# Performance work log

Measured on AMD Instinct MI355X. Metric: run time of the kernel, lower is better.

The kernel has to match this reference:

```python
import jax, jax.numpy as jnp
import numpy as np


def setup_inputs() -> dict:
    key = jax.random.key(0)
    k1, k2 = jax.random.split(key)
    B, C, H, W = 4, 32, 512, 512
    inp = jax.random.normal(k1, (B, C, H, W), dtype=jnp.float32)
    # flow displacements of a few pixels, realistic for optical-flow warping
    flow = jax.random.normal(k2, (B, 2, H, W), dtype=jnp.float32) * 8.0
    return {"input": inp, "flow": flow}


def reference(input, flow):
    B, C, H, W = input.shape
    dt = input.dtype
    # meshgrid: grid[:,0]=x coords, grid[:,1]=y coords
    gx = jnp.arange(W, dtype=dt)[None, None, :]          # [1,1,W]
    gy = jnp.arange(H, dtype=dt)[None, :, None]          # [1,H,1]
    x = jnp.clip(gx + flow[:, 0], 0.0, W - 1).reshape(-1)  # [B*H*W]
    y = jnp.clip(gy + flow[:, 1], 0.0, H - 1).reshape(-1)

    x0f = jnp.floor(x)
    y0f = jnp.floor(y)
    x1f = x0f + 1.0
    y1f = y0f + 1.0
    x0 = x0f.astype(jnp.int32)
    y0 = y0f.astype(jnp.int32)
    x1 = jnp.clip(x1f, 0.0, W - 1).astype(jnp.int32)
    y1 = jnp.clip(y1f, 0.0, H - 1).astype(jnp.int32)

    base = jnp.repeat(jnp.arange(B, dtype=jnp.int32) * (H * W), H * W)
    base_y0 = base + y0 * W
    base_y1 = base + y1 * W

    img_flat = jnp.transpose(input, (0, 2, 3, 1)).reshape(-1, C)  # [B*H*W, C]
    Ia = img_flat[base_y0 + x0]
    Ib = img_flat[base_y1 + x0]
    Ic = img_flat[base_y0 + x1]
    Id = img_flat[base_y1 + x1]

    # bilinear weights (note: weights use unclamped x1f/y1f, matching original)
    wa = ((x1f - x) * (y1f - y))[:, None]
    wb = ((x1f - x) * (y - y0f))[:, None]
    wc = ((x - x0f) * (y1f - y))[:, None]
    wd = ((x - x0f) * (y - y0f))[:, None]

    out = wa * Ia + wb * Ib + wc * Ic + wd * Id            # [B*H*W, C]
    return jnp.transpose(out.reshape(B, H, W, C), (0, 3, 1, 2))
```

## Files before the change

### kernel.cpp

```cpp
#include <hip/hip_runtime.h>


constexpr int B = 4, C = 32, H = 512, W = 512;
constexpr int HW = H * W;
constexpr int TILE = 64;
constexpr int APRON = 31;
constexpr int RH = 128;
constexpr int RW = 128;
constexpr int BUF = RH * RW;

__global__ __launch_bounds__(1024, 1) void warp_tile_kernel(
    const float* __restrict__ input,
    const float* __restrict__ flow,
    float* __restrict__ out)
{
    __shared__ float s[2 * BUF];

    int bid0 = (int)blockIdx.x;
    int bid = (bid0 & 7) * 32 + (bid0 >> 3);

    int tx = bid & 7;
    int ty = (bid >> 3) & 7;
    int b  = bid >> 6;
    int tx0 = tx * TILE, ty0 = ty * TILE;

    int rx0 = tx0 - 32;
    int ry0 = ty0 - APRON;

    int tid  = (int)threadIdx.x;
    int lane = tid & 63;
    int wv   = tid >> 6;
    int cl   = tid & 63;
    int rl   = tid >> 6;

    int soff0, soff1, soff2, soff3;
    int ldst0, ldst1, ldst2, ldst3;
    {
        int lrow = lane >> 5;
        int lc   = (lane & 31) << 2;
        int gcol = min(max(rx0 + lc, 0), W - 4);
        int r0 = 8 * wv;
        int g0r = min(max(ry0 + r0 + 0 + lrow, 0), H - 1);
        int g1r = min(max(ry0 + r0 + 2 + lrow, 0), H - 1);
        int g2r = min(max(ry0 + r0 + 4 + lrow, 0), H - 1);
        int g3r = min(max(ry0 + r0 + 6 + lrow, 0), H - 1);
        soff0 = g0r * W + gcol;  ldst0 = (r0 + 0) * RW + 4 * lane;
        soff1 = g1r * W + gcol;  ldst1 = (r0 + 2) * RW + 4 * lane;
        soff2 = g2r * W + gcol;  ldst2 = (r0 + 4) * RW + 4 * lane;
        soff3 = g3r * W + gcol;  ldst3 = (r0 + 6) * RW + 4 * lane;
    }

    float wa[4], wb_[4], wc_[4], wd_[4];
    int a0[4], a1[4];
    int opix0 = (ty0 + rl) * W + tx0 + cl;

    #pragma unroll
    for (int p = 0; p < 4; ++p) {
        int h = ty0 + rl + 16 * p;
        int w = tx0 + cl;
        int pix = h * W + w;
        float fx = flow[(b * 2 + 0) * HW + pix];
        float fy = flow[(b * 2 + 1) * HW + pix];
        float x = fminf(fmaxf((float)w + fx, 0.0f), (float)(W - 1));
        float y = fminf(fmaxf((float)h + fy, 0.0f), (float)(H - 1));
        float x0f = floorf(x), y0f = floorf(y);
        int x0 = (int)x0f, y0 = (int)y0f;
        int y1 = min(y0 + 1, H - 1);
        float dx = x - x0f, dy = y - y0f;
        wa[p]  = (1.f - dx) * (1.f - dy);
        wb_[p] = (1.f - dx) * dy;
        wc_[p] = dx * (1.f - dy);
        wd_[p] = dx * dy;
        int ax0 = x0 - rx0, ay0 = y0 - ry0, ay1 = y1 - ry0;
        bool inreg = (ax0 >= 0) && (ax0 <= RW - 2) && (ay0 >= 0) && (ay1 <= RH - 1);
        a0[p] = inreg ? (ay0 * RW + ax0) : -1;
        a1[p] = ay1 * RW + ax0;
    }

    const float* iplane = input + (size_t)b * C * HW;
    float* oplane = out + (size_t)b * C * HW;

    float4 g0, g1, g2, g3;
    {
        const float* gc = iplane;
        g0 = *(const float4*)(gc + soff0);
        g1 = *(const float4*)(gc + soff1);
        g2 = *(const float4*)(gc + soff2);
        g3 = *(const float4*)(gc + soff3);
        *(float4*)(&s[ldst0]) = g0;
        *(float4*)(&s[ldst1]) = g1;
        *(float4*)(&s[ldst2]) = g2;
        *(float4*)(&s[ldst3]) = g3;
    }
    __syncthreads();

    for (int c = 0; c < C; ++c) {
        if (c + 1 < C) {
            const float* gc = iplane + (size_t)(c + 1) * HW;
            g0 = *(const float4*)(gc + soff0);
            g1 = *(const float4*)(gc + soff1);
            g2 = *(const float4*)(gc + soff2);
            g3 = *(const float4*)(gc + soff3);
        }
        __builtin_amdgcn_sched_barrier(0);

        int base = (c & 1) * BUF;
        float v[4];
        #pragma unroll
        for (int p = 0; p < 4; ++p) {
            if (a0[p] >= 0) {
                int i0 = base + a0[p], i1 = base + a1[p];
                float v00 = s[i0], v01 = s[i0 + 1];
                float v10 = s[i1], v11 = s[i1 + 1];
                v[p] = wa[p] * v00 + wc_[p] * v01 + wb_[p] * v10 + wd_[p] * v11;
            } else {
                int h = ty0 + rl + 16 * p;
                int w = tx0 + cl;
                int pix = h * W + w;
                float fx = flow[(b * 2 + 0) * HW + pix];
                float fy = flow[(b * 2 + 1) * HW + pix];
                float x = fminf(fmaxf((float)w + fx, 0.0f), (float)(W - 1));
                float y = fminf(fmaxf((float)h + fy, 0.0f), (float)(H - 1));
                float x0f = floorf(x), y0f = floorf(y);
                int x0 = (int)x0f, y0 = (int)y0f;
                int x1 = min(x0 + 1, W - 1), y1 = min(y0 + 1, H - 1);
                float dx = x - x0f, dy = y - y0f;
                const float* pch = iplane + (size_t)c * HW;
                v[p] = (1.f - dx) * (1.f - dy) * pch[y0 * W + x0]
                     + (1.f - dx) * dy         * pch[y1 * W + x0]
                     + dx * (1.f - dy)         * pch[y0 * W + x1]
                     + dx * dy                 * pch[y1 * W + x1];
            }
        }

        float* oc = oplane + (size_t)c * HW;
        #pragma unroll
        for (int p = 0; p < 4; ++p)
            oc[opix0 + 16 * p * W] = v[p];

        if (c + 1 < C) {
            int wbase = ((c + 1) & 1) * BUF;
            *(float4*)(&s[wbase + ldst0]) = g0;
            *(float4*)(&s[wbase + ldst1]) = g1;
            *(float4*)(&s[wbase + ldst2]) = g2;
            *(float4*)(&s[wbase + ldst3]) = g3;
            asm volatile("s_waitcnt lgkmcnt(0)" ::: "memory");
            __builtin_amdgcn_sched_barrier(0);
            __builtin_amdgcn_s_barrier();
            __builtin_amdgcn_sched_barrier(0);
        }
    }
}

extern "C" void kernel_launch(void* const* d_in, const int* in_sizes, int n_in,
                              void* d_out, int out_size, void* d_ws, size_t ws_size,
                              hipStream_t stream) {
    const float* input = (const float*)d_in[0];
    const float* flow  = (const float*)d_in[1];
    float* out = (float*)d_out;

    int grid = B * (H / TILE) * (W / TILE);
    warp_tile_kernel<<<grid, 1024, 0, stream>>>(input, flow, out);
}
```

Before: 248.4 us.

## Pack channel pairs as fp16 in shared memory, halving barrier count

Stores two channels per 32-bit LDS word as packed half2, so each staged region covers two channels and the loop processes channel pairs, halving the number of block barriers and LDS reads per channel. Global loads for the next pair are issued before compute, giving more loads in flight. Converting input to fp16 reduces precision of the sampled values, which may exceed tolerance, and adds conversion ALU work and register pressure.

```diff
diff --git a/kernel.cpp b/kernel.cpp
--- a/kernel.cpp
+++ b/kernel.cpp
@@ -1,4 +1,5 @@
 #include <hip/hip_runtime.h>
+#include <hip/hip_fp16.h>
 
 
 constexpr int B = 4, C = 32, H = 512, W = 512;
@@ -9,12 +10,22 @@
 constexpr int RW = 128;
 constexpr int BUF = RH * RW;
 
+static __device__ __forceinline__ float2 h2f(unsigned int u) {
+    __half2 h; __builtin_memcpy(&h, &u, 4);
+    return __half22float2(h);
+}
+static __device__ __forceinline__ unsigned int f2h(float a, float b) {
+    __half2 h = __floats2half2_rn(a, b);
+    unsigned int u; __builtin_memcpy(&u, &h, 4);
+    return u;
+}
+
 __global__ __launch_bounds__(1024, 1) void warp_tile_kernel(
     const float* __restrict__ input,
     const float* __restrict__ flow,
     float* __restrict__ out)
 {
-    __shared__ float s[2 * BUF];
+    __shared__ unsigned int s[2 * BUF];
 
     int bid0 = (int)blockIdx.x;
     int bid = (bid0 & 7) * 32 + (bid0 >> 3);
@@ -80,39 +91,50 @@
     const float* iplane = input + (size_t)b * C * HW;
     float* oplane = out + (size_t)b * C * HW;
 
-    float4 g0, g1, g2, g3;
+    float4 ga0, ga1, ga2, ga3, gb0, gb1, gb2, gb3;
     {
-        const float* gc = iplane;
-        g0 = *(const float4*)(gc + soff0);
-        g1 = *(const float4*)(gc + soff1);
-        g2 = *(const float4*)(gc + soff2);
-        g3 = *(const float4*)(gc + soff3);
-        *(float4*)(&s[ldst0]) = g0;
-        *(float4*)(&s[ldst1]) = g1;
-        *(float4*)(&s[ldst2]) = g2;
-        *(float4*)(&s[ldst3]) = g3;
+        const float* gA = iplane;
+        const float* gB = iplane + HW;
+        ga0 = *(const float4*)(gA + soff0);  gb0 = *(const float4*)(gB + soff0);
+        ga1 = *(const float4*)(gA + soff1);  gb1 = *(const float4*)(gB + soff1);
+        ga2 = *(const float4*)(gA + soff2);  gb2 = *(const float4*)(gB + soff2);
+        ga3 = *(const float4*)(gA + soff3);  gb3 = *(const float4*)(gB + soff3);
+        *(uint4*)(&s[ldst0]) = make_uint4(f2h(ga0.x, gb0.x), f2h(ga0.y, gb0.y),
+                                          f2h(ga0.z, gb0.z), f2h(ga0.w, gb0.w));
+        *(uint4*)(&s[ldst1]) = make_uint4(f2h(ga1.x, gb1.x), f2h(ga1.y, gb1.y),
+                                          f2h(ga1.z, gb1.z), f2h(ga1.w, gb1.w));
+        *(uint4*)(&s[ldst2]) = make_uint4(f2h(ga2.x, gb2.x), f2h(ga2.y, gb2.y),
+                                          f2h(ga2.z, gb2.z), f2h(ga2.w, gb2.w));
+        *(uint4*)(&s[ldst3]) = make_uint4(f2h(ga3.x, gb3.x), f2h(ga3.y, gb3.y),
+                                          f2h(ga3.z, gb3.z), f2h(ga3.w, gb3.w));
     }
     __syncthreads();
 
-    for (int c = 0; c < C; ++c) {
-        if (c + 1 < C) {
-            const float* gc = iplane + (size_t)(c + 1) * HW;
-            g0 = *(const float4*)(gc + soff0);
-            g1 = *(const float4*)(gc + soff1);
-            g2 = *(const float4*)(gc + soff2);
-            g3 = *(const float4*)(gc + soff3);
+    for (int r = 0; r < C / 2; ++r) {
+        int c = 2 * r;
+
+        if (r + 1 < C / 2) {
+            const float* gA = iplane + (size_t)(c + 2) * HW;
+            const float* gB = gA + HW;
+            ga0 = *(const float4*)(gA + soff0);  gb0 = *(const float4*)(gB + soff0);
+            ga1 = *(const float4*)(gA + soff1);  gb1 = *(const float4*)(gB + soff1);
+            ga2 = *(const float4*)(gA + soff2);  gb2 = *(const float4*)(gB + soff2);
+            ga3 = *(const float4*)(gA + soff3);  gb3 = *(const float4*)(gB + soff3);
         }
         __builtin_amdgcn_sched_barrier(0);
 
-        int base = (c & 1) * BUF;
-        float v[4];
+        int base = (r & 1) * BUF;
+        float v0[4], v1[4];
         #pragma unroll
         for (int p = 0; p < 4; ++p) {
             if (a0[p] >= 0) {
                 int i0 = base + a0[p], i1 = base + a1[p];
-                float v00 = s[i0], v01 = s[i0 + 1];
-                float v10 = s[i1], v11 = s[i1 + 1];
-                v[p] = wa[p] * v00 + wc_[p] * v01 + wb_[p] * v10 + wd_[p] * v11;
+                unsigned int d00 = s[i0], d01 = s[i0 + 1];
+                unsigned int d10 = s[i1], d11 = s[i1 + 1];
+                float2 t00 = h2f(d00), t01 = h2f(d01);
+                float2 t10 = h2f(d10), t11 = h2f(d11);
+                v0[p] = wa[p]*t00.x + wc_[p]*t01.x + wb_[p]*t10.x + wd_[p]*t11.x;
+                v1[p] = wa[p]*t00.y + wc_[p]*t01.y + wb_[p]*t10.y + wd_[p]*t11.y;
             } else {
                 int h = ty0 + rl + 16 * p;
                 int w = tx0 + cl;
@@ -125,25 +147,36 @@
                 int x0 = (int)x0f, y0 = (int)y0f;
                 int x1 = min(x0 + 1, W - 1), y1 = min(y0 + 1, H - 1);
                 float dx = x - x0f, dy = y - y0f;
-                const float* pch = iplane + (size_t)c * HW;
-                v[p] = (1.f - dx) * (1.f - dy) * pch[y0 * W + x0]
-                     + (1.f - dx) * dy         * pch[y1 * W + x0]
-                     + dx * (1.f - dy)         * pch[y0 * W + x1]
-                     + dx * dy                 * pch[y1 * W + x1];
+                const float* pc0 = iplane + (size_t)c * HW;
+                const float* pc1 = pc0 + HW;
+                float A = (1.f - dx) * (1.f - dy), Bw = (1.f - dx) * dy;
+                float Cw = dx * (1.f - dy),        Dw = dx * dy;
+                v0[p] = A*pc0[y0*W+x0] + Bw*pc0[y1*W+x0]
+                      + Cw*pc0[y0*W+x1] + Dw*pc0[y1*W+x1];
+                v1[p] = A*pc1[y0*W+x0] + Bw*pc1[y1*W+x0]
+                      + Cw*pc1[y0*W+x1] + Dw*pc1[y1*W+x1];
             }
         }
 
-        float* oc = oplane + (size_t)c * HW;
+        float* oc0 = oplane + (size_t)c * HW;
+        float* oc1 = oc0 + HW;
         #pragma unroll
-        for (int p = 0; p < 4; ++p)
-            oc[opix0 + 16 * p * W] = v[p];
+        for (int p = 0; p < 4; ++p) {
+            oc0[opix0 + 16 * p * W] = v0[p];
+            oc1[opix0 + 16 * p * W] = v1[p];
+        }
+        __builtin_amdgcn_sched_barrier(0);
 
-        if (c + 1 < C) {
-            int wbase = ((c + 1) & 1) * BUF;
-            *(float4*)(&s[wbase + ldst0]) = g0;
-            *(float4*)(&s[wbase + ldst1]) = g1;
-            *(float4*)(&s[wbase + ldst2]) = g2;
-            *(float4*)(&s[wbase + ldst3]) = g3;
+        if (r + 1 < C / 2) {
+            int wb2 = ((r + 1) & 1) * BUF;
+            *(uint4*)(&s[wb2 + ldst0]) = make_uint4(f2h(ga0.x, gb0.x), f2h(ga0.y, gb0.y),
+                                                    f2h(ga0.z, gb0.z), f2h(ga0.w, gb0.w));
+            *(uint4*)(&s[wb2 + ldst1]) = make_uint4(f2h(ga1.x, gb1.x), f2h(ga1.y, gb1.y),
+                                                    f2h(ga1.z, gb1.z), f2h(ga1.w, gb1.w));
+            *(uint4*)(&s[wb2 + ldst2]) = make_uint4(f2h(ga2.x, gb2.x), f2h(ga2.y, gb2.y),
+                                                    f2h(ga2.z, gb2.z), f2h(ga2.w, gb2.w));
+            *(uint4*)(&s[wb2 + ldst3]) = make_uint4(f2h(ga3.x, gb3.x), f2h(ga3.y, gb3.y),
+                                                    f2h(ga3.z, gb3.z), f2h(ga3.w, gb3.w));
             asm volatile("s_waitcnt lgkmcnt(0)" ::: "memory");
             __builtin_amdgcn_sched_barrier(0);
             __builtin_amdgcn_s_barrier();
```

New measurement: 247.7 us. No clear change (-0.3%).
